# Kernel optimization log

Hardware: AMD Instinct MI355X
Metric: run time of the kernel (lower is better)

## Reference

```python
import jax, jax.numpy as jnp
import numpy as np

N = 16384      # bs(2048) * n_agents(8)
D_IN = 256     # input_shape
H = 256        # rnn_hidden_dim
E = 256        # hypernet_embed
A = 32         # n_actions


def setup_inputs() -> dict:
    key = jax.random.key(0)
    ks = jax.random.split(key, 18)
    s = 0.05
    f32 = jnp.float32
    return {
        "x": jax.random.normal(ks[0], (N, D_IN), f32),
        "h": jax.random.normal(ks[1], (N, H), f32) * 0.1,
        "fc1_w": jax.random.normal(ks[2], (D_IN, H), f32) * s,
        "fc1_b": jnp.zeros((H,), f32),
        "gru_w_ih": jax.random.normal(ks[3], (H, 3 * H), f32) * s,
        "gru_b_ih": jnp.zeros((3 * H,), f32),
        "gru_w_hh": jax.random.normal(ks[4], (H, 3 * H), f32) * s,
        "gru_b_hh": jnp.zeros((3 * H,), f32),
        "hg_w1": jax.random.normal(ks[5], (H, E), f32) * s,
        "hg_b1": jnp.zeros((E,), f32),
        "hg_w2": jax.random.normal(ks[6], (E, E), f32) * s,
        "hg_b2": jnp.zeros((E,), f32),
        "hb_w": jax.random.normal(ks[7], (E, A), f32) * s,
        "hb_b": jnp.zeros((A,), f32),
        "hw_w": jax.random.normal(ks[8], (E, H * A), f32) * s,
        "hw_b": jnp.zeros((H * A,), f32),
    }


def _gru_cell(x, h, w_ih, b_ih, w_hh, b_hh):
    # torch.nn.GRUCell semantics (gate order: r, z, n)
    gi = x @ w_ih + b_ih            # [N, 3H]
    gh = h @ w_hh + b_hh            # [N, 3H]
    i_r, i_z, i_n = jnp.split(gi, 3, axis=-1)
    h_r, h_z, h_n = jnp.split(gh, 3, axis=-1)
    r = jax.nn.sigmoid(i_r + h_r)
    z = jax.nn.sigmoid(i_z + h_z)
    n = jnp.tanh(i_n + r * h_n)
    return (1.0 - z) * n + z * h


def reference(x, h, fc1_w, fc1_b, gru_w_ih, gru_b_ih, gru_w_hh, gru_b_hh,
              hg_w1, hg_b1, hg_w2, hg_b2, hb_w, hb_b, hw_w, hw_b):
    x1 = jax.nn.relu(x @ fc1_w + fc1_b)                       # [N, H]
    hn = _gru_cell(x1, h, gru_w_ih, gru_b_ih, gru_w_hh, gru_b_hh)  # [N, H]
    # hypernet latent
    g = jnp.tanh(jax.nn.relu(hn @ hg_w1 + hg_b1) @ hg_w2 + hg_b2)  # [N, E]
    b_dyn = g @ hb_w + hb_b                                    # [N, A]
    w_dyn = (g @ hw_w + hw_b).reshape(hn.shape[0], H, A)       # [N, H, A]
    q = jnp.einsum('nh,nha->na', hn, w_dyn) + b_dyn            # [N, A]
    return q
```

## Files before the change

### kernel.cpp

```cpp
#include <hip/hip_runtime.h>


typedef _Float16 half8 __attribute__((ext_vector_type(8)));
typedef _Float16 half4 __attribute__((ext_vector_type(4)));
typedef float f32x4 __attribute__((ext_vector_type(4)));

#define MFMA16(a, b, c) __builtin_amdgcn_mfma_f32_16x16x32_f16((a), (b), (c), 0, 0, 0)

constexpr int NROWS = 16384;

__device__ __forceinline__ float sigmoidf_(float x) { return 1.0f / (1.0f + __expf(-x)); }

__device__ __forceinline__ void glds16(const void* g, void* l) {
    __builtin_amdgcn_global_load_lds((const __attribute__((address_space(1))) void*)g,
                                     (__attribute__((address_space(3))) void*)l, 16, 0, 0);
}

__global__ void cvt_kernel(const float* __restrict__ x, const float* __restrict__ h,
                           _Float16* __restrict__ x16, _Float16* __restrict__ xh) {
    int b = blockIdx.x;
    if (b < 4096) {
        int i = (b * 256 + threadIdx.x) * 4;
        float4 v = *reinterpret_cast<const float4*>(x + i);
        x16[i + 0] = (_Float16)v.x; x16[i + 1] = (_Float16)v.y;
        x16[i + 2] = (_Float16)v.z; x16[i + 3] = (_Float16)v.w;
    } else {
        int i = ((b - 4096) * 256 + threadIdx.x) * 4;
        float4 v = *reinterpret_cast<const float4*>(h + i);
        int n = i >> 8, j = i & 255;
        _Float16* o = xh + n * 512 + 256 + j;
        o[0] = (_Float16)v.x; o[1] = (_Float16)v.y;
        o[2] = (_Float16)v.z; o[3] = (_Float16)v.w;
    }
}

__global__ void wtrans_kernel(const float* __restrict__ s0, const float* __restrict__ s1,
                              const float* __restrict__ s2, const float* __restrict__ s3,
                              const float* __restrict__ s4, _Float16* __restrict__ d0,
                              _Float16* __restrict__ d1, _Float16* __restrict__ d2,
                              _Float16* __restrict__ d3, _Float16* __restrict__ d4) {
    __shared__ float tile[32][33];
    int b = blockIdx.x;
    const float* src; _Float16* dst; int C, idx;
    if (b < 64)       { src = s0; dst = d0; C = 256;  idx = b; }
    else if (b < 128) { src = s1; dst = d1; C = 256;  idx = b - 64; }
    else if (b < 192) { src = s2; dst = d2; C = 256;  idx = b - 128; }
    else if (b < 200) { src = s3; dst = d3; C = 32;   idx = b - 192; }
    else              { src = s4; dst = d4; C = 8192; idx = b - 200; }
    int kb = (idx & 7) * 32, cb = (idx >> 3) * 32;
    int tx = threadIdx.x, ty = threadIdx.y;
#pragma unroll
    for (int i = ty; i < 32; i += 8) tile[i][tx] = src[(kb + i) * C + cb + tx];
    __syncthreads();
#pragma unroll
    for (int i = ty; i < 32; i += 8) {
        int c = cb + i, k = kb + tx;
        dst[c * 256 + (k ^ ((c & 7) << 3))] = (_Float16)tile[tx][i];
    }
}

__global__ void wgru_prep_kernel(const float* __restrict__ gwih, const float* __restrict__ gwhh,
                                 _Float16* __restrict__ wgru) {
    __shared__ float tile[32][33];
    int b = blockIdx.x, job = b >> 6, idx = b & 63;
    int kb = (idx & 7) * 32, cb = (idx >> 3) * 32;
    const float* src = (job & 1) ? gwhh : gwih;
    int coff = (job >> 1) * 256;
    int gate = (job < 4) ? (job >> 1) : (2 + (job & 1));
    int koff = (job & 1) * 256;
    int tx = threadIdx.x, ty = threadIdx.y;
#pragma unroll
    for (int i = ty; i < 32; i += 8) tile[i][tx] = src[(kb + i) * 768 + coff + cb + tx];
    __syncthreads();
#pragma unroll
    for (int i = ty; i < 32; i += 8) {
        int c = cb + i;
        int row = (c >> 4) * 64 + gate * 16 + (c & 15);
        int kk = kb + tx + koff;
        wgru[row * 512 + (kk ^ ((row & 7) << 3))] = (_Float16)tile[tx][i];
    }
}

template <int ACT>
__global__ __launch_bounds__(256, 2) void gemm_lds_kernel(
    const _Float16* __restrict__ Am, const _Float16* __restrict__ Wt,
    const float* __restrict__ bias, _Float16* __restrict__ out16, int ONC) {
    __shared__ _Float16 Bs[64 * 256];
    const int tid = threadIdx.x, wave = tid >> 6, lane = tid & 63;
    const int r = lane & 15, kg = lane >> 4;
    const int row0 = blockIdx.x * 256 + wave * 64;
    const int col0 = blockIdx.y * 64;
    const _Float16* src = Wt + col0 * 256;
#pragma unroll
    for (int it = 0; it < 8; ++it)
        glds16(src + it * 2048 + tid * 8, Bs + it * 2048 + tid * 8);
    asm volatile("s_waitcnt vmcnt(0)" ::: "memory");
    __syncthreads();

    f32x4 z = {0.f, 0.f, 0.f, 0.f};
    f32x4 acc[4][4];
#pragma unroll
    for (int t = 0; t < 4; t++)
#pragma unroll
        for (int j = 0; j < 4; j++) acc[t][j] = z;
    const int swz = (r & 7) << 4;
#pragma unroll
    for (int kb = 0; kb < 8; kb++) {
        half8 a[4], bm[4];
#pragma unroll
        for (int t = 0; t < 4; t++)
            a[t] = *reinterpret_cast<const half8*>(Am + (row0 + t * 16 + r) * 256 + kb * 32 + kg * 8);
#pragma unroll
        for (int j = 0; j < 4; j++)
            bm[j] = *reinterpret_cast<const half8*>(
                (const char*)Bs + (j * 16 + r) * 512 + ((kb * 64 + kg * 16) ^ swz));
#pragma unroll
        for (int t = 0; t < 4; t++)
#pragma unroll
            for (int j = 0; j < 4; j++) acc[t][j] = MFMA16(a[t], bm[j], acc[t][j]);
    }
#pragma unroll
    for (int j = 0; j < 4; j++) {
        int cc = col0 + j * 16 + r;
        float bv = bias[cc];
#pragma unroll
        for (int t = 0; t < 4; t++)
#pragma unroll
            for (int i = 0; i < 4; i++) {
                int rr = row0 + t * 16 + kg * 4 + i;
                float v = acc[t][j][i] + bv;
                if (ACT == 1) v = fmaxf(v, 0.0f);
                if (ACT == 2) v = tanhf(v);
                out16[rr * ONC + cc] = (_Float16)v;
            }
    }
}

__global__ __launch_bounds__(256, 2) void gru_kernel(
    const _Float16* __restrict__ xh, const float* __restrict__ hf,
    const _Float16* __restrict__ wgru, const float* __restrict__ bih,
    const float* __restrict__ bhh, _Float16* __restrict__ hn16) {
    __shared__ _Float16 Bs[64 * 512];
    const int tid = threadIdx.x, wave = tid >> 6, lane = tid & 63;
    const int r = lane & 15, kg = lane >> 4;
    const int row0 = blockIdx.x * 256 + wave * 64;
    const int c0 = blockIdx.y * 16;
    const _Float16* src = wgru + (size_t)blockIdx.y * 64 * 512;
#pragma unroll
    for (int it = 0; it < 16; ++it)
        glds16(src + it * 2048 + tid * 8, Bs + it * 2048 + tid * 8);
    asm volatile("s_waitcnt vmcnt(0)" ::: "memory");
    __syncthreads();

    f32x4 z = {0.f, 0.f, 0.f, 0.f};
    f32x4 acc[4][4];
#pragma unroll
    for (int t = 0; t < 4; t++)
#pragma unroll
        for (int j = 0; j < 4; j++) acc[t][j] = z;
    const int swz = (r & 7) << 4;
#pragma unroll
    for (int kb = 0; kb < 16; kb++) {
        half8 a[4], bm[4];
#pragma unroll
        for (int t = 0; t < 4; t++)
            a[t] = *reinterpret_cast<const half8*>(xh + (row0 + t * 16 + r) * 512 + kb * 32 + kg * 8);
#pragma unroll
        for (int j = 0; j < 4; j++)
            bm[j] = *reinterpret_cast<const half8*>(
                (const char*)Bs + (j * 16 + r) * 1024 + ((kb * 64 + kg * 16) ^ swz));
#pragma unroll
        for (int t = 0; t < 4; t++)
#pragma unroll
            for (int j = 0; j < 4; j++) acc[t][j] = MFMA16(a[t], bm[j], acc[t][j]);
    }
    const int cc = c0 + r;
    float brz = bih[cc] + bhh[cc];
    float bzz = bih[256 + cc] + bhh[256 + cc];
    float bin = bih[512 + cc], bhn = bhh[512 + cc];
#pragma unroll
    for (int t = 0; t < 4; t++)
#pragma unroll
        for (int i = 0; i < 4; i++) {
            int rr = row0 + t * 16 + kg * 4 + i;
            float rg = sigmoidf_(acc[t][0][i] + brz);
            float zg = sigmoidf_(acc[t][1][i] + bzz);
            float nn = tanhf(acc[t][2][i] + bin + rg * (acc[t][3][i] + bhn));
            float v = (1.0f - zg) * nn + zg * hf[rr * 256 + cc];
            hn16[rr * 256 + cc] = (_Float16)v;
        }
}

__global__ void hnt_kernel(const _Float16* __restrict__ hn16, _Float16* __restrict__ hnT16) {
    __shared__ float tile[32][33];
    int r0 = blockIdx.x * 32, c0 = blockIdx.y * 32;
    int tx = threadIdx.x, ty = threadIdx.y;
#pragma unroll
    for (int i = ty; i < 32; i += 8) tile[i][tx] = (float)hn16[(r0 + i) * 256 + c0 + tx];
    __syncthreads();
#pragma unroll
    for (int i = ty; i < 32; i += 8)
        hnT16[(size_t)(c0 + i) * NROWS + r0 + tx] = (_Float16)tile[tx][i];
}

__global__ __launch_bounds__(256)
__attribute__((amdgpu_waves_per_eu(2, 2))) void final_kernel(
    const _Float16* __restrict__ g16, const _Float16* __restrict__ hwt,
    const float* __restrict__ hwb, const _Float16* __restrict__ hbt,
    const float* __restrict__ hbb, const _Float16* __restrict__ hnT16,
    float* __restrict__ q) {
    __shared__ _Float16 Bs[3][8192];
    __shared__ _Float16 hvs[8192];
    __shared__ float hwbs[1024];
    const int bid = blockIdx.x;
    const int by = bid & 7, bx = bid >> 3;
    const int tid = threadIdx.x, wave = tid >> 6, lane = tid & 63;
    const int r = lane & 15, kg = lane >> 4;
    const int row0 = bx * 256 + wave * 64;
    const int hbase = by * 32;
    const int swz = (r & 7) << 4;

#pragma unroll
    for (int it = 0; it < 4; ++it) {
        int e = it * 2048 + tid * 8;
        glds16(hnT16 + (size_t)(hbase + (e >> 8)) * NROWS + bx * 256 + (e & 255), hvs + e);
    }
    glds16(hwb + hbase * 32 + tid * 4, hwbs + tid * 4);
#pragma unroll
    for (int it = 0; it < 4; ++it) {
        int e = it * 2048 + tid * 8;
        glds16(hwt + (size_t)hbase * 8192 + e, &Bs[0][0] + e);
    }
#pragma unroll
    for (int it = 0; it < 4; ++it) {
        int e = it * 2048 + tid * 8;
        glds16(hwt + (size_t)(hbase + 1) * 8192 + e, &Bs[1][0] + e);
    }

    half8 ga[4][8];
#pragma unroll
    for (int t = 0; t < 4; t++)
#pragma unroll
        for (int kb = 0; kb < 8; kb++) {
            ga[t][kb] = *reinterpret_cast<const half8*>(
                g16 + (row0 + t * 16 + r) * 256 + kb * 32 + kg * 8);
            asm volatile("" : "+v"(ga[t][kb]));
        }

    f32x4 qa[4][2];
    if (by == 0) {
        float b0v = hbb[r], b1v = hbb[16 + r];
#pragma unroll
        for (int t = 0; t < 4; t++) {
            qa[t][0] = {b0v, b0v, b0v, b0v};
            qa[t][1] = {b1v, b1v, b1v, b1v};
        }
#pragma unroll
        for (int kb = 0; kb < 8; kb++) {
            const int c0b = (kb * 64 + kg * 16) ^ swz;
            half8 hb0 = *reinterpret_cast<const half8*>((const char*)hbt + r * 512 + c0b);
            half8 hb1 = *reinterpret_cast<const half8*>((const char*)hbt + (16 + r) * 512 + c0b);
#pragma unroll
            for (int t = 0; t < 4; t++) {
                qa[t][0] = MFMA16(ga[t][kb], hb0, qa[t][0]);
                qa[t][1] = MFMA16(ga[t][kb], hb1, qa[t][1]);
            }
        }
    } else {
        f32x4 z = {0.f, 0.f, 0.f, 0.f};
#pragma unroll
        for (int t = 0; t < 4; t++) { qa[t][0] = z; qa[t][1] = z; }
    }

    int cur = 0;
    for (int h = 0; h < 32; ++h) {
        if (h < 30)
            asm volatile("s_waitcnt vmcnt(4)" ::: "memory");
        else
            asm volatile("s_waitcnt vmcnt(0)" ::: "memory");
        __builtin_amdgcn_s_barrier();
        if (h < 30) {
            int pre = cur + 2; if (pre >= 3) pre -= 3;
            const _Float16* src = hwt + (size_t)(hbase + h + 2) * 8192;
            _Float16* dst = &Bs[pre][0];
#pragma unroll
            for (int it = 0; it < 4; ++it) {
                int e = it * 2048 + tid * 8;
                glds16(src + e, dst + e);
            }
        }
        const char* bp = (const char*)&Bs[cur][0];
        float wb0 = hwbs[h * 32 + r], wb1 = hwbs[h * 32 + 16 + r];
        f32x4 w[4][2];
#pragma unroll
        for (int t = 0; t < 4; t++) {
            w[t][0] = {wb0, wb0, wb0, wb0};
            w[t][1] = {wb1, wb1, wb1, wb1};
        }
#pragma unroll
        for (int kb = 0; kb < 8; kb++) {
            const int c0b = (kb * 64 + kg * 16) ^ swz;
            half8 b0 = *reinterpret_cast<const half8*>(bp + r * 512 + c0b);
            half8 b1 = *reinterpret_cast<const half8*>(bp + (16 + r) * 512 + c0b);
#pragma unroll
            for (int t = 0; t < 4; t++) {
                w[t][0] = MFMA16(ga[t][kb], b0, w[t][0]);
                w[t][1] = MFMA16(ga[t][kb], b1, w[t][1]);
            }
        }
#pragma unroll
        for (int t = 0; t < 4; t++) {
            half4 hv4 = *reinterpret_cast<const half4*>(hvs + h * 256 + wave * 64 + t * 16 + kg * 4);
#pragma unroll
            for (int i = 0; i < 4; i++) {
                float hvf = (float)hv4[i];
                qa[t][0][i] += hvf * w[t][0][i];
                qa[t][1][i] += hvf * w[t][1][i];
            }
        }
        cur = cur + 1; if (cur >= 3) cur -= 3;
    }

#pragma unroll
    for (int t = 0; t < 4; t++)
#pragma unroll
        for (int i = 0; i < 4; i++) {
            int rr = row0 + t * 16 + kg * 4 + i;
            atomicAdd(&q[rr * 32 + r], qa[t][0][i]);
            atomicAdd(&q[rr * 32 + 16 + r], qa[t][1][i]);
        }
}

extern "C" void kernel_launch(void* const* d_in, const int* in_sizes, int n_in,
                              void* d_out, int out_size, void* d_ws, size_t ws_size,
                              hipStream_t stream) {
    const float* x = (const float*)d_in[0];
    const float* h = (const float*)d_in[1];
    const float* fc1_w = (const float*)d_in[2];
    const float* fc1_b = (const float*)d_in[3];
    const float* gwih = (const float*)d_in[4];
    const float* gbih = (const float*)d_in[5];
    const float* gwhh = (const float*)d_in[6];
    const float* gbhh = (const float*)d_in[7];
    const float* hgw1 = (const float*)d_in[8];
    const float* hgb1 = (const float*)d_in[9];
    const float* hgw2 = (const float*)d_in[10];
    const float* hgb2 = (const float*)d_in[11];
    const float* hbw = (const float*)d_in[12];
    const float* hbb = (const float*)d_in[13];
    const float* hww = (const float*)d_in[14];
    const float* hwb = (const float*)d_in[15];
    float* q = (float*)d_out;

    char* p = (char*)d_ws;
    auto alloc = [&](size_t bytes) { char* r = p; p += (bytes + 255) & ~255ULL; return r; };
    _Float16* x16 = (_Float16*)alloc((size_t)NROWS * 256 * 2);
    _Float16* xh = (_Float16*)alloc((size_t)NROWS * 512 * 2);
    _Float16* w1t = (_Float16*)alloc((size_t)256 * 256 * 2);
    _Float16* wgru = (_Float16*)alloc((size_t)1024 * 512 * 2);
    _Float16* hg1t = (_Float16*)alloc((size_t)256 * 256 * 2);
    _Float16* hg2t = (_Float16*)alloc((size_t)256 * 256 * 2);
    _Float16* hbt = (_Float16*)alloc((size_t)32 * 256 * 2);
    _Float16* hwt = (_Float16*)alloc((size_t)8192 * 256 * 2);
    _Float16* hn16 = (_Float16*)alloc((size_t)NROWS * 256 * 2);
    _Float16* hnT16 = (_Float16*)alloc((size_t)256 * NROWS * 2);
    _Float16* t16 = (_Float16*)alloc((size_t)NROWS * 256 * 2);
    _Float16* g16 = (_Float16*)alloc((size_t)NROWS * 256 * 2);

    cvt_kernel<<<8192, 256, 0, stream>>>(x, h, x16, xh);
    wtrans_kernel<<<2248, dim3(32, 8), 0, stream>>>(fc1_w, hgw1, hgw2, hbw, hww,
                                                    w1t, hg1t, hg2t, hbt, hwt);
    hipMemsetAsync(wgru, 0, (size_t)1024 * 512 * 2, stream);
    wgru_prep_kernel<<<384, dim3(32, 8), 0, stream>>>(gwih, gwhh, wgru);

    hipMemsetAsync(d_out, 0, (size_t)NROWS * 32 * sizeof(float), stream);

    gemm_lds_kernel<1><<<dim3(64, 4), 256, 0, stream>>>(x16, w1t, fc1_b, xh, 512);

    gru_kernel<<<dim3(64, 16), 256, 0, stream>>>(xh, h, wgru, gbih, gbhh, hn16);
    hnt_kernel<<<dim3(512, 8), dim3(32, 8), 0, stream>>>(hn16, hnT16);

    gemm_lds_kernel<1><<<dim3(64, 4), 256, 0, stream>>>(hn16, hg1t, hgb1, t16, 256);
    gemm_lds_kernel<2><<<dim3(64, 4), 256, 0, stream>>>(t16, hg2t, hgb2, g16, 256);

    final_kernel<<<512, 256, 0, stream>>>(g16, hwt, hwb, hbt, hbb, hnT16, q);
}
```

Baseline: 184.1 us.

## Double per-wave row tile to 128 rows across GEMM, GRU and final kernels

Each wave now computes 128 rows instead of 64 in the gemm, GRU and final kernels, which halves grid sizes and doubles how often each LDS-staged weight tile is reused. The final kernel also simplifies the hb bias GEMM to a single k-block per by-slice and splits the hw columns into two passes to limit live accumulators. The cost is much higher register pressure, with waves_per_eu dropped to 1, and fewer blocks (128 or 256) on a 256-CU GPU, which lowers occupancy and latency hiding.

```diff
diff --git a/kernel.cpp b/kernel.cpp
--- a/kernel.cpp
+++ b/kernel.cpp
@@ -88,7 +88,7 @@
     __shared__ _Float16 Bs[64 * 256];
     const int tid = threadIdx.x, wave = tid >> 6, lane = tid & 63;
     const int r = lane & 15, kg = lane >> 4;
-    const int row0 = blockIdx.x * 256 + wave * 64;
+    const int row0 = blockIdx.x * 512 + wave * 128;
     const int col0 = blockIdx.y * 64;
     const _Float16* src = Wt + col0 * 256;
 #pragma unroll
@@ -98,24 +98,24 @@
     __syncthreads();
 
     f32x4 z = {0.f, 0.f, 0.f, 0.f};
-    f32x4 acc[4][4];
-#pragma unroll
-    for (int t = 0; t < 4; t++)
+    f32x4 acc[8][4];
+#pragma unroll
+    for (int t = 0; t < 8; t++)
 #pragma unroll
         for (int j = 0; j < 4; j++) acc[t][j] = z;
     const int swz = (r & 7) << 4;
 #pragma unroll
     for (int kb = 0; kb < 8; kb++) {
-        half8 a[4], bm[4];
-#pragma unroll
-        for (int t = 0; t < 4; t++)
+        half8 a[8], bm[4];
+#pragma unroll
+        for (int t = 0; t < 8; t++)
             a[t] = *reinterpret_cast<const half8*>(Am + (row0 + t * 16 + r) * 256 + kb * 32 + kg * 8);
 #pragma unroll
         for (int j = 0; j < 4; j++)
             bm[j] = *reinterpret_cast<const half8*>(
                 (const char*)Bs + (j * 16 + r) * 512 + ((kb * 64 + kg * 16) ^ swz));
 #pragma unroll
-        for (int t = 0; t < 4; t++)
+        for (int t = 0; t < 8; t++)
 #pragma unroll
             for (int j = 0; j < 4; j++) acc[t][j] = MFMA16(a[t], bm[j], acc[t][j]);
     }
@@ -124,7 +124,7 @@
         int cc = col0 + j * 16 + r;
         float bv = bias[cc];
 #pragma unroll
-        for (int t = 0; t < 4; t++)
+        for (int t = 0; t < 8; t++)
 #pragma unroll
             for (int i = 0; i < 4; i++) {
                 int rr = row0 + t * 16 + kg * 4 + i;
@@ -143,7 +143,7 @@
     __shared__ _Float16 Bs[64 * 512];
     const int tid = threadIdx.x, wave = tid >> 6, lane = tid & 63;
     const int r = lane & 15, kg = lane >> 4;
-    const int row0 = blockIdx.x * 256 + wave * 64;
+    const int row0 = blockIdx.x * 512 + wave * 128;
     const int c0 = blockIdx.y * 16;
     const _Float16* src = wgru + (size_t)blockIdx.y * 64 * 512;
 #pragma unroll
@@ -153,24 +153,24 @@
     __syncthreads();
 
     f32x4 z = {0.f, 0.f, 0.f, 0.f};
-    f32x4 acc[4][4];
-#pragma unroll
-    for (int t = 0; t < 4; t++)
+    f32x4 acc[8][4];
+#pragma unroll
+    for (int t = 0; t < 8; t++)
 #pragma unroll
         for (int j = 0; j < 4; j++) acc[t][j] = z;
     const int swz = (r & 7) << 4;
 #pragma unroll
     for (int kb = 0; kb < 16; kb++) {
-        half8 a[4], bm[4];
-#pragma unroll
-        for (int t = 0; t < 4; t++)
+        half8 a[8], bm[4];
+#pragma unroll
+        for (int t = 0; t < 8; t++)
             a[t] = *reinterpret_cast<const half8*>(xh + (row0 + t * 16 + r) * 512 + kb * 32 + kg * 8);
 #pragma unroll
         for (int j = 0; j < 4; j++)
             bm[j] = *reinterpret_cast<const half8*>(
                 (const char*)Bs + (j * 16 + r) * 1024 + ((kb * 64 + kg * 16) ^ swz));
 #pragma unroll
-        for (int t = 0; t < 4; t++)
+        for (int t = 0; t < 8; t++)
 #pragma unroll
             for (int j = 0; j < 4; j++) acc[t][j] = MFMA16(a[t], bm[j], acc[t][j]);
     }
@@ -179,7 +179,7 @@
     float bzz = bih[256 + cc] + bhh[256 + cc];
     float bin = bih[512 + cc], bhn = bhh[512 + cc];
 #pragma unroll
-    for (int t = 0; t < 4; t++)
+    for (int t = 0; t < 8; t++)
 #pragma unroll
         for (int i = 0; i < 4; i++) {
             int rr = row0 + t * 16 + kg * 4 + i;
@@ -204,26 +204,38 @@
 }
 
 __global__ __launch_bounds__(256)
-__attribute__((amdgpu_waves_per_eu(2, 2))) void final_kernel(
+__attribute__((amdgpu_waves_per_eu(1, 1))) void final_kernel(
     const _Float16* __restrict__ g16, const _Float16* __restrict__ hwt,
     const float* __restrict__ hwb, const _Float16* __restrict__ hbt,
     const float* __restrict__ hbb, const _Float16* __restrict__ hnT16,
     float* __restrict__ q) {
     __shared__ _Float16 Bs[3][8192];
-    __shared__ _Float16 hvs[8192];
+    __shared__ _Float16 hvs[16384];
     __shared__ float hwbs[1024];
     const int bid = blockIdx.x;
     const int by = bid & 7, bx = bid >> 3;
     const int tid = threadIdx.x, wave = tid >> 6, lane = tid & 63;
     const int r = lane & 15, kg = lane >> 4;
-    const int row0 = bx * 256 + wave * 64;
+    const int row0 = bx * 512 + wave * 128;
     const int hbase = by * 32;
     const int swz = (r & 7) << 4;
 
-#pragma unroll
-    for (int it = 0; it < 4; ++it) {
+    half8 ga[8][8];
+#pragma unroll
+    for (int t = 0; t < 8; t++)
+#pragma unroll
+        for (int kb = 0; kb < 8; kb++)
+            ga[t][kb] = *reinterpret_cast<const half8*>(
+                g16 + (row0 + t * 16 + r) * 256 + kb * 32 + kg * 8);
+
+    const int cby = (by * 64 + kg * 16) ^ swz;
+    half8 hb0 = *reinterpret_cast<const half8*>((const char*)hbt + r * 512 + cby);
+    half8 hb1 = *reinterpret_cast<const half8*>((const char*)hbt + (16 + r) * 512 + cby);
+
+#pragma unroll
+    for (int it = 0; it < 8; ++it) {
         int e = it * 2048 + tid * 8;
-        glds16(hnT16 + (size_t)(hbase + (e >> 8)) * NROWS + bx * 256 + (e & 255), hvs + e);
+        glds16(hnT16 + (size_t)(hbase + (e >> 9)) * NROWS + bx * 512 + (e & 511), hvs + e);
     }
     glds16(hwb + hbase * 32 + tid * 4, hwbs + tid * 4);
 #pragma unroll
@@ -237,39 +249,26 @@
         glds16(hwt + (size_t)(hbase + 1) * 8192 + e, &Bs[1][0] + e);
     }
 
-    half8 ga[4][8];
-#pragma unroll
-    for (int t = 0; t < 4; t++)
-#pragma unroll
-        for (int kb = 0; kb < 8; kb++) {
-            ga[t][kb] = *reinterpret_cast<const half8*>(
-                g16 + (row0 + t * 16 + r) * 256 + kb * 32 + kg * 8);
+#pragma unroll
+    for (int t = 0; t < 8; t++)
+#pragma unroll
+        for (int kb = 0; kb < 8; kb++)
             asm volatile("" : "+v"(ga[t][kb]));
-        }
-
-    f32x4 qa[4][2];
-    if (by == 0) {
-        float b0v = hbb[r], b1v = hbb[16 + r];
-#pragma unroll
-        for (int t = 0; t < 4; t++) {
+
+    f32x4 qa[8][2];
+    {
+        float b0v = (by == 0) ? hbb[r] : 0.0f;
+        float b1v = (by == 0) ? hbb[16 + r] : 0.0f;
+#pragma unroll
+        for (int t = 0; t < 8; t++) {
             qa[t][0] = {b0v, b0v, b0v, b0v};
             qa[t][1] = {b1v, b1v, b1v, b1v};
         }
 #pragma unroll
-        for (int kb = 0; kb < 8; kb++) {
-            const int c0b = (kb * 64 + kg * 16) ^ swz;
-            half8 hb0 = *reinterpret_cast<const half8*>((const char*)hbt + r * 512 + c0b);
-            half8 hb1 = *reinterpret_cast<const half8*>((const char*)hbt + (16 + r) * 512 + c0b);
-#pragma unroll
-            for (int t = 0; t < 4; t++) {
-                qa[t][0] = MFMA16(ga[t][kb], hb0, qa[t][0]);
-                qa[t][1] = MFMA16(ga[t][kb], hb1, qa[t][1]);
-            }
-        }
-    } else {
-        f32x4 z = {0.f, 0.f, 0.f, 0.f};
-#pragma unroll
-        for (int t = 0; t < 4; t++) { qa[t][0] = z; qa[t][1] = z; }
+        for (int t = 0; t < 8; t++) {
+            qa[t][0] = MFMA16(ga[t][by], hb0, qa[t][0]);
+            qa[t][1] = MFMA16(ga[t][by], hb1, qa[t][1]);
+        }
     }
 
     int cur = 0;
@@ -290,39 +289,32 @@
             }
         }
         const char* bp = (const char*)&Bs[cur][0];
-        float wb0 = hwbs[h * 32 + r], wb1 = hwbs[h * 32 + 16 + r];
-        f32x4 w[4][2];
-#pragma unroll
-        for (int t = 0; t < 4; t++) {
-            w[t][0] = {wb0, wb0, wb0, wb0};
-            w[t][1] = {wb1, wb1, wb1, wb1};
-        }
-#pragma unroll
-        for (int kb = 0; kb < 8; kb++) {
-            const int c0b = (kb * 64 + kg * 16) ^ swz;
-            half8 b0 = *reinterpret_cast<const half8*>(bp + r * 512 + c0b);
-            half8 b1 = *reinterpret_cast<const half8*>(bp + (16 + r) * 512 + c0b);
-#pragma unroll
-            for (int t = 0; t < 4; t++) {
-                w[t][0] = MFMA16(ga[t][kb], b0, w[t][0]);
-                w[t][1] = MFMA16(ga[t][kb], b1, w[t][1]);
+#pragma unroll
+        for (int c = 0; c < 2; ++c) {
+            float wb = hwbs[(h << 5) + (c << 4) + r];
+            f32x4 w[8];
+#pragma unroll
+            for (int t = 0; t < 8; t++) w[t] = {wb, wb, wb, wb};
+#pragma unroll
+            for (int kb = 0; kb < 8; kb++) {
+                half8 b = *reinterpret_cast<const half8*>(
+                    bp + (c * 16 + r) * 512 + ((kb * 64 + kg * 16) ^ swz));
+#pragma unroll
+                for (int t = 0; t < 8; t++) w[t] = MFMA16(ga[t][kb], b, w[t]);
             }
-        }
-#pragma unroll
-        for (int t = 0; t < 4; t++) {
-            half4 hv4 = *reinterpret_cast<const half4*>(hvs + h * 256 + wave * 64 + t * 16 + kg * 4);
-#pragma unroll
-            for (int i = 0; i < 4; i++) {
-                float hvf = (float)hv4[i];
-                qa[t][0][i] += hvf * w[t][0][i];
-                qa[t][1][i] += hvf * w[t][1][i];
+#pragma unroll
+            for (int t = 0; t < 8; t++) {
+                half4 hv4 = *reinterpret_cast<const half4*>(
+                    hvs + (h << 9) + wave * 128 + t * 16 + kg * 4);
+#pragma unroll
+                for (int i = 0; i < 4; i++) qa[t][c][i] += (float)hv4[i] * w[t][i];
             }
         }
         cur = cur + 1; if (cur >= 3) cur -= 3;
     }
 
 #pragma unroll
-    for (int t = 0; t < 4; t++)
+    for (int t = 0; t < 8; t++)
 #pragma unroll
         for (int i = 0; i < 4; i++) {
             int rr = row0 + t * 16 + kg * 4 + i;
@@ -375,13 +367,13 @@
 
     hipMemsetAsync(d_out, 0, (size_t)NROWS * 32 * sizeof(float), stream);
 
-    gemm_lds_kernel<1><<<dim3(64, 4), 256, 0, stream>>>(x16, w1t, fc1_b, xh, 512);
-
-    gru_kernel<<<dim3(64, 16), 256, 0, stream>>>(xh, h, wgru, gbih, gbhh, hn16);
+    gemm_lds_kernel<1><<<dim3(32, 4), 256, 0, stream>>>(x16, w1t, fc1_b, xh, 512);
+
+    gru_kernel<<<dim3(32, 16), 256, 0, stream>>>(xh, h, wgru, gbih, gbhh, hn16);
     hnt_kernel<<<dim3(512, 8), dim3(32, 8), 0, stream>>>(hn16, hnT16);
 
-    gemm_lds_kernel<1><<<dim3(64, 4), 256, 0, stream>>>(hn16, hg1t, hgb1, t16, 256);
-    gemm_lds_kernel<2><<<dim3(64, 4), 256, 0, stream>>>(t16, hg2t, hgb2, g16, 256);
-
-    final_kernel<<<512, 256, 0, stream>>>(g16, hwt, hwb, hbt, hbb, hnT16, q);
-}
+    gemm_lds_kernel<1><<<dim3(32, 4), 256, 0, stream>>>(hn16, hg1t, hgb1, t16, 256);
+    gemm_lds_kernel<2><<<dim3(32, 4), 256, 0, stream>>>(t16, hg2t, hgb2, g16, 256);
+
+    final_kernel<<<256, 256, 0, stream>>>(g16, hwt, hwb, hbt, hbb, hnT16, q);
+}
```

After: 258.2 us. +40.2%, slower.

## Fuse hn transpose into GRU epilogue and double-buffer final kernel for occupancy

Applied to the files above, without the earlier changes.

The GRU kernel now writes its fp16 output tile into shared memory and stores the transposed hn directly, which removes the separate hnt_kernel launch and its extra read of hn16. The final kernel goes from a triple to a double LDS buffer, with a full wait and barrier on every iteration and launch bounds raised to 3 blocks per SIMD for more occupancy. It also raises wave priority around the MFMA block. The trade-off is less prefetch depth and a full memory drain each step in exchange for more resident waves.

```diff
diff --git a/kernel.cpp b/kernel.cpp
--- a/kernel.cpp
+++ b/kernel.cpp
@@ -139,7 +139,8 @@
 __global__ __launch_bounds__(256, 2) void gru_kernel(
     const _Float16* __restrict__ xh, const float* __restrict__ hf,
     const _Float16* __restrict__ wgru, const float* __restrict__ bih,
-    const float* __restrict__ bhh, _Float16* __restrict__ hn16) {
+    const float* __restrict__ bhh, _Float16* __restrict__ hn16,
+    _Float16* __restrict__ hnT16) {
     __shared__ _Float16 Bs[64 * 512];
     const int tid = threadIdx.x, wave = tid >> 6, lane = tid & 63;
     const int r = lane & 15, kg = lane >> 4;
@@ -178,6 +179,7 @@
     float brz = bih[cc] + bhh[cc];
     float bzz = bih[256 + cc] + bhh[256 + cc];
     float bin = bih[512 + cc], bhn = bhh[512 + cc];
+    _Float16 vs[4][4];
 #pragma unroll
     for (int t = 0; t < 4; t++)
 #pragma unroll
@@ -187,29 +189,34 @@
             float zg = sigmoidf_(acc[t][1][i] + bzz);
             float nn = tanhf(acc[t][2][i] + bin + rg * (acc[t][3][i] + bhn));
             float v = (1.0f - zg) * nn + zg * hf[rr * 256 + cc];
-            hn16[rr * 256 + cc] = (_Float16)v;
-        }
-}
-
-__global__ void hnt_kernel(const _Float16* __restrict__ hn16, _Float16* __restrict__ hnT16) {
-    __shared__ float tile[32][33];
-    int r0 = blockIdx.x * 32, c0 = blockIdx.y * 32;
-    int tx = threadIdx.x, ty = threadIdx.y;
-#pragma unroll
-    for (int i = ty; i < 32; i += 8) tile[i][tx] = (float)hn16[(r0 + i) * 256 + c0 + tx];
-    __syncthreads();
-#pragma unroll
-    for (int i = ty; i < 32; i += 8)
-        hnT16[(size_t)(c0 + i) * NROWS + r0 + tx] = (_Float16)tile[tx][i];
-}
-
-__global__ __launch_bounds__(256)
-__attribute__((amdgpu_waves_per_eu(2, 2))) void final_kernel(
+            _Float16 v16 = (_Float16)v;
+            hn16[rr * 256 + cc] = v16;
+            vs[t][i] = v16;
+        }
+    __syncthreads();
+    _Float16* tile = Bs;
+#pragma unroll
+    for (int t = 0; t < 4; t++)
+#pragma unroll
+        for (int i = 0; i < 4; i++)
+            tile[r * 264 + wave * 64 + t * 16 + kg * 4 + i] = vs[t][i];
+    __syncthreads();
+    {
+        int trow = tid >> 4, chunk = tid & 15;
+        half8 v0 = *reinterpret_cast<const half8*>(tile + trow * 264 + chunk * 16);
+        half8 v1 = *reinterpret_cast<const half8*>(tile + trow * 264 + chunk * 16 + 8);
+        size_t dst = (size_t)(c0 + trow) * NROWS + blockIdx.x * 256 + chunk * 16;
+        *reinterpret_cast<half8*>(hnT16 + dst) = v0;
+        *reinterpret_cast<half8*>(hnT16 + dst + 8) = v1;
+    }
+}
+
+__global__ __launch_bounds__(256, 3) void final_kernel(
     const _Float16* __restrict__ g16, const _Float16* __restrict__ hwt,
     const float* __restrict__ hwb, const _Float16* __restrict__ hbt,
     const float* __restrict__ hbb, const _Float16* __restrict__ hnT16,
     float* __restrict__ q) {
-    __shared__ _Float16 Bs[3][8192];
+    __shared__ _Float16 Bs[2][8192];
     __shared__ _Float16 hvs[8192];
     __shared__ float hwbs[1024];
     const int bid = blockIdx.x;
@@ -220,23 +227,6 @@
     const int hbase = by * 32;
     const int swz = (r & 7) << 4;
 
-#pragma unroll
-    for (int it = 0; it < 4; ++it) {
-        int e = it * 2048 + tid * 8;
-        glds16(hnT16 + (size_t)(hbase + (e >> 8)) * NROWS + bx * 256 + (e & 255), hvs + e);
-    }
-    glds16(hwb + hbase * 32 + tid * 4, hwbs + tid * 4);
-#pragma unroll
-    for (int it = 0; it < 4; ++it) {
-        int e = it * 2048 + tid * 8;
-        glds16(hwt + (size_t)hbase * 8192 + e, &Bs[0][0] + e);
-    }
-#pragma unroll
-    for (int it = 0; it < 4; ++it) {
-        int e = it * 2048 + tid * 8;
-        glds16(hwt + (size_t)(hbase + 1) * 8192 + e, &Bs[1][0] + e);
-    }
-
     half8 ga[4][8];
 #pragma unroll
     for (int t = 0; t < 4; t++)
@@ -247,6 +237,18 @@
             asm volatile("" : "+v"(ga[t][kb]));
         }
 
+#pragma unroll
+    for (int it = 0; it < 4; ++it) {
+        int e = it * 2048 + tid * 8;
+        glds16(hnT16 + (size_t)(hbase + (e >> 8)) * NROWS + bx * 256 + (e & 255), hvs + e);
+    }
+    glds16(hwb + hbase * 32 + tid * 4, hwbs + tid * 4);
+#pragma unroll
+    for (int it = 0; it < 4; ++it) {
+        int e = it * 2048 + tid * 8;
+        glds16(hwt + (size_t)hbase * 8192 + e, &Bs[0][0] + e);
+    }
+
     f32x4 qa[4][2];
     if (by == 0) {
         float b0v = hbb[r], b1v = hbb[16 + r];
@@ -272,31 +274,28 @@
         for (int t = 0; t < 4; t++) { qa[t][0] = z; qa[t][1] = z; }
     }
 
-    int cur = 0;
+    asm volatile("s_waitcnt vmcnt(0) lgkmcnt(0)" ::: "memory");
+    __builtin_amdgcn_s_barrier();
+
     for (int h = 0; h < 32; ++h) {
-        if (h < 30)
-            asm volatile("s_waitcnt vmcnt(4)" ::: "memory");
-        else
-            asm volatile("s_waitcnt vmcnt(0)" ::: "memory");
-        __builtin_amdgcn_s_barrier();
-        if (h < 30) {
-            int pre = cur + 2; if (pre >= 3) pre -= 3;
-            const _Float16* src = hwt + (size_t)(hbase + h + 2) * 8192;
-            _Float16* dst = &Bs[pre][0];
+        if (h < 31) {
+            const _Float16* src = hwt + (size_t)(hbase + h + 1) * 8192;
+            _Float16* dst = &Bs[(h + 1) & 1][0];
 #pragma unroll
             for (int it = 0; it < 4; ++it) {
                 int e = it * 2048 + tid * 8;
                 glds16(src + e, dst + e);
             }
         }
-        const char* bp = (const char*)&Bs[cur][0];
-        float wb0 = hwbs[h * 32 + r], wb1 = hwbs[h * 32 + 16 + r];
+        const char* bp = (const char*)&Bs[h & 1][0];
+        float wb0 = hwbs[(h << 5) + r], wb1 = hwbs[(h << 5) + 16 + r];
         f32x4 w[4][2];
 #pragma unroll
         for (int t = 0; t < 4; t++) {
             w[t][0] = {wb0, wb0, wb0, wb0};
             w[t][1] = {wb1, wb1, wb1, wb1};
         }
+        __builtin_amdgcn_s_setprio(1);
 #pragma unroll
         for (int kb = 0; kb < 8; kb++) {
             const int c0b = (kb * 64 + kg * 16) ^ swz;
@@ -308,9 +307,10 @@
                 w[t][1] = MFMA16(ga[t][kb], b1, w[t][1]);
             }
         }
+        __builtin_amdgcn_s_setprio(0);
 #pragma unroll
         for (int t = 0; t < 4; t++) {
-            half4 hv4 = *reinterpret_cast<const half4*>(hvs + h * 256 + wave * 64 + t * 16 + kg * 4);
+            half4 hv4 = *reinterpret_cast<const half4*>(hvs + (h << 8) + wave * 64 + t * 16 + kg * 4);
 #pragma unroll
             for (int i = 0; i < 4; i++) {
                 float hvf = (float)hv4[i];
@@ -318,7 +318,8 @@
                 qa[t][1][i] += hvf * w[t][1][i];
             }
         }
-        cur = cur + 1; if (cur >= 3) cur -= 3;
+        asm volatile("s_waitcnt vmcnt(0) lgkmcnt(0)" ::: "memory");
+        __builtin_amdgcn_s_barrier();
     }
 
 #pragma unroll
@@ -377,8 +378,7 @@
 
     gemm_lds_kernel<1><<<dim3(64, 4), 256, 0, stream>>>(x16, w1t, fc1_b, xh, 512);
 
-    gru_kernel<<<dim3(64, 16), 256, 0, stream>>>(xh, h, wgru, gbih, gbhh, hn16);
-    hnt_kernel<<<dim3(512, 8), dim3(32, 8), 0, stream>>>(hn16, hnT16);
+    gru_kernel<<<dim3(64, 16), 256, 0, stream>>>(xh, h, wgru, gbih, gbhh, hn16, hnT16);
 
     gemm_lds_kernel<1><<<dim3(64, 4), 256, 0, stream>>>(hn16, hg1t, hgb1, t16, 256);
     gemm_lds_kernel<2><<<dim3(64, 4), 256, 0, stream>>>(t16, hg2t, hgb2, g16, 256);
```

Result: slower. 299.8 us (+62.8%).
